# Kernel optimization log

Measured on AMD Instinct MI355X. Metric: run time of the kernel, lower is better.

## Reference

```python
import jax, jax.numpy as jnp
import numpy as np

HIDDEN = 768
HEADS = 12
HEAD_DIM = HIDDEN // HEADS
LN_EPS = 1e-5


def setup_inputs() -> dict:
    key = jax.random.key(0)
    ks = jax.random.split(key, 12)
    B, S, H = 8, 1024, HIDDEN
    s = 1.0 / np.sqrt(H)
    inputs = jax.random.normal(ks[0], (B, S, H), dtype=jnp.float32)
    adj = jax.random.randint(ks[1], (B, S, S), 0, 2, dtype=jnp.int32)
    Wq = jax.random.uniform(ks[2], (H, H), jnp.float32, -s, s)
    bq = jax.random.uniform(ks[3], (H,), jnp.float32, -s, s)
    Wk = jax.random.uniform(ks[4], (H, H), jnp.float32, -s, s)
    bk = jax.random.uniform(ks[5], (H,), jnp.float32, -s, s)
    Wv = jax.random.uniform(ks[6], (H, H), jnp.float32, -s, s)
    bv = jax.random.uniform(ks[7], (H,), jnp.float32, -s, s)
    Wo = jax.random.uniform(ks[8], (H, H), jnp.float32, -s, s)
    bo = jax.random.uniform(ks[9], (H,), jnp.float32, -s, s)
    gamma = jnp.ones((H,), jnp.float32)
    beta = jnp.zeros((H,), jnp.float32)
    return {"inputs": inputs, "adj": adj, "Wq": Wq, "bq": bq, "Wk": Wk,
            "bk": bk, "Wv": Wv, "bv": bv, "Wo": Wo, "bo": bo,
            "gamma": gamma, "beta": beta}


def reference(inputs, adj, Wq, bq, Wk, bk, Wv, bv, Wo, bo, gamma, beta):
    B, S, H = inputs.shape
    def heads(x):  # [B,S,H] -> [B,heads,S,head_dim]
        return x.reshape(B, S, HEADS, HEAD_DIM).transpose(0, 2, 1, 3)
    Q = heads(inputs @ Wq.T + bq)
    K = heads(inputs @ Wk.T + bk)
    V = heads(inputs @ Wv.T + bv)
    scores = jnp.einsum('bhqd,bhkd->bhqk', Q, K) / np.sqrt(HEAD_DIM)
    mask = (adj[:, None, :, :] == 0)  # [B,1,S,S] broadcast over heads
    scores = jnp.where(mask, jnp.float32(-1e9), scores)
    attn = jax.nn.softmax(scores, axis=-1)
    # dropout is identity in eval mode
    ctx = jnp.einsum('bhqk,bhkd->bhqd', attn, V)
    ctx = ctx.transpose(0, 2, 1, 3).reshape(B, S, H)
    out = ctx @ Wo.T + bo
    x = out + inputs
    mu = jnp.mean(x, axis=-1, keepdims=True)
    var = jnp.mean(jnp.square(x - mu), axis=-1, keepdims=True)
    return (x - mu) * jax.lax.rsqrt(var + LN_EPS) * gamma + beta
```

## Files before the change

### kernel.cpp

```cpp
#include <hip/hip_runtime.h>

typedef __bf16 bf16_t;
typedef __bf16 bf16x8 __attribute__((ext_vector_type(8)));
typedef float f32x4 __attribute__((ext_vector_type(4)));
typedef unsigned short u16;

__device__ __forceinline__ u16 f2bf(float f) {
  unsigned u = __float_as_uint(f);
  unsigned r = (u + 0x7fffu + ((u >> 16) & 1u)) >> 16;
  return (u16)r;
}
__device__ __forceinline__ float bf2f(u16 u) {
  return __uint_as_float(((unsigned)u) << 16);
}

typedef const unsigned __attribute__((address_space(1)))* gptr_t;
typedef unsigned __attribute__((address_space(3)))* lptr_t;

__device__ __forceinline__ void gload_lds16(const u16* g, u16* l) {
  __builtin_amdgcn_global_load_lds((gptr_t)(const void*)g, (lptr_t)(void*)l, 16, 0, 0);
}

#define QSCALE 0.18033688f
#define EPS 136

__global__ __launch_bounds__(256) void cvt_f32_bf16(const float* __restrict__ in,
                                                    u16* __restrict__ out, int n4) {
  int i = blockIdx.x * 256 + threadIdx.x;
  if (i >= n4) return;
  float4 v = reinterpret_cast<const float4*>(in)[i];
  ushort4 o;
  o.x = f2bf(v.x); o.y = f2bf(v.y); o.z = f2bf(v.z); o.w = f2bf(v.w);
  reinterpret_cast<ushort4*>(out)[i] = o;
}

__global__ __launch_bounds__(256) void cvt_w4(const float* __restrict__ Wq,
                                              const float* __restrict__ Wk,
                                              const float* __restrict__ Wv,
                                              const float* __restrict__ Wo,
                                              u16* __restrict__ out) {
  int sel = blockIdx.y;
  const float* in = sel == 0 ? Wq : sel == 1 ? Wk : sel == 2 ? Wv : Wo;
  u16* o = out + sel * 589824;
  int i = blockIdx.x * 256 + threadIdx.x;
  float4 v = reinterpret_cast<const float4*>(in)[i];
  ushort4 ov;
  ov.x = f2bf(v.x); ov.y = f2bf(v.y); ov.z = f2bf(v.z); ov.w = f2bf(v.w);
  reinterpret_cast<ushort4*>(o)[i] = ov;
}

__global__ __launch_bounds__(256) void pack_adj(const int* __restrict__ adj,
                                                unsigned* __restrict__ bits) {
  unsigned idx = blockIdx.x * 256u + threadIdx.x;
  int a = adj[idx];
  unsigned long long m = __ballot(a != 0);
  int l = threadIdx.x & 63;
  if ((l & 31) == 0) bits[idx >> 5] = (unsigned)(m >> (l & 32));
}


__global__ __launch_bounds__(256, 4) void gemm_qkv(
    const u16* __restrict__ A,
    const u16* __restrict__ Wq, const u16* __restrict__ Wk, const u16* __restrict__ Wv,
    const float* __restrict__ bq, const float* __restrict__ bk, const float* __restrict__ bv,
    u16* __restrict__ Qo, u16* __restrict__ Ko, u16* __restrict__ Vo) {
  __shared__ u16 lds[2][2][128 * 32];
  const int tid = threadIdx.x;
  const int w = tid >> 6, l = tid & 63;
  const int bm = blockIdx.x;
  const int bn = blockIdx.y;
  const int sel = bn / 6;
  const int bnl = bn % 6;
  const int lr = l & 15, lg = l >> 4;
  const int wm = w >> 1, wn = w & 1;

  const u16* W = sel == 0 ? Wq : sel == 1 ? Wk : Wv;
  const float* bias = sel == 0 ? bq : sel == 1 ? bk : bv;

  const u16* Abase = A + (bm * 128) * 768;
  const u16* Wbase = W + (bnl * 128) * 768;

  const int c0 = tid, c1 = tid + 256;
  const int sr0 = c0 >> 3, pg0 = c0 & 7, g0 = pg0 ^ (sr0 & 7);
  const int off0 = (2 * sr0 + (g0 >> 2)) * 768 + (g0 & 3) * 8;
  const int sr1 = c1 >> 3, pg1 = c1 & 7, g1 = pg1 ^ (sr1 & 7);
  const int off1 = (2 * sr1 + (g1 >> 2)) * 768 + (g1 & 3) * 8;

  int aoff[4], boff[4];
#pragma unroll
  for (int i = 0; i < 4; ++i) {
    int R = wm * 64 + i * 16 + lr, sr = R >> 1;
    int g = (R & 1) * 4 + lg, pg = g ^ (sr & 7);
    aoff[i] = sr * 64 + pg * 8;
    R = wn * 64 + i * 16 + lr; sr = R >> 1;
    g = (R & 1) * 4 + lg; pg = g ^ (sr & 7);
    boff[i] = sr * 64 + pg * 8;
  }

  f32x4 acc[4][4];
#pragma unroll
  for (int i = 0; i < 4; ++i)
#pragma unroll
    for (int j = 0; j < 4; ++j) acc[i][j] = f32x4{0.f, 0.f, 0.f, 0.f};

  auto stage = [&](int buf, int k0) {
    gload_lds16(Abase + off0 + k0, &lds[buf][0][c0 * 8]);
    gload_lds16(Abase + off1 + k0, &lds[buf][0][c1 * 8]);
    gload_lds16(Wbase + off0 + k0, &lds[buf][1][c0 * 8]);
    gload_lds16(Wbase + off1 + k0, &lds[buf][1][c1 * 8]);
  };

  stage(0, 0);
  int cur = 0;
  for (int kt = 0; kt < 24; ++kt) {
    __syncthreads();
    if (kt < 23) stage(cur ^ 1, (kt + 1) * 32);
    const u16* la = &lds[cur][0][0];
    const u16* lb = &lds[cur][1][0];
    bf16x8 af[4], bw[4];
#pragma unroll
    for (int i = 0; i < 4; ++i) af[i] = *(const bf16x8*)&la[aoff[i]];
#pragma unroll
    for (int j = 0; j < 4; ++j) bw[j] = *(const bf16x8*)&lb[boff[j]];
#pragma unroll
    for (int i = 0; i < 4; ++i)
#pragma unroll
      for (int j = 0; j < 4; ++j)
        acc[i][j] = __builtin_amdgcn_mfma_f32_16x16x32_bf16(af[i], bw[j], acc[i][j], 0, 0, 0);
    cur ^= 1;
  }

  __syncthreads();
  u16* ep = &lds[0][0][0];
  const int n0 = bnl * 128 + wn * 64;

  if (sel != 2) {
    const float sc = sel == 0 ? QSCALE : 1.0f;
    u16* dst = sel == 0 ? Qo : Ko;
#pragma unroll
    for (int p = 0; p < 2; ++p) {
      if (wm == p) {
#pragma unroll
        for (int j = 0; j < 4; ++j) {
          float bs = bias[n0 + j * 16 + lr];
#pragma unroll
          for (int i = 0; i < 4; ++i)
#pragma unroll
            for (int r = 0; r < 4; ++r)
              ep[(i * 16 + lg * 4 + r) * EPS + wn * 64 + j * 16 + lr] =
                  f2bf((acc[i][j][r] + bs) * sc);
        }
      }
      __syncthreads();
#pragma unroll
      for (int it = 0; it < 4; ++it) {
        int u = it * 256 + tid, row = u >> 4, cc = u & 15;
        uint4 val = *(const uint4*)&ep[row * EPS + cc * 8];
        int m = bm * 128 + p * 64 + row;
        int b_ = m >> 10, s_ = m & 1023;
        int h_ = (bnl * 128 + cc * 8) >> 6, d_ = (cc & 7) * 8;
        *(uint4*)&dst[((b_ * 12 + h_) * 1024 + s_) * 64 + d_] = val;
      }
      __syncthreads();
    }
  } else {
#pragma unroll
    for (int p = 0; p < 2; ++p) {
      if (wn == p) {
#pragma unroll
        for (int j = 0; j < 4; ++j) {
          float bs = bias[n0 + j * 16 + lr];
#pragma unroll
          for (int i = 0; i < 4; ++i) {
            ushort4 o4;
            o4.x = f2bf(acc[i][j][0] + bs);
            o4.y = f2bf(acc[i][j][1] + bs);
            o4.z = f2bf(acc[i][j][2] + bs);
            o4.w = f2bf(acc[i][j][3] + bs);
            *(ushort4*)&ep[(j * 16 + lr) * EPS + wm * 64 + i * 16 + lg * 4] = o4;
          }
        }
      }
      __syncthreads();
#pragma unroll
      for (int it = 0; it < 4; ++it) {
        int u = it * 256 + tid, row = u >> 4, cc = u & 15;
        uint4 val = *(const uint4*)&ep[row * EPS + cc * 8];
        int dg = bnl * 128 + p * 64 + row;
        int h_ = dg >> 6, d_ = dg & 63;
        int b_ = bm >> 3, s_ = (bm & 7) * 128 + cc * 8;
        *(uint4*)&Vo[((b_ * 12 + h_) * 64 + d_) * 1024 + s_] = val;
      }
      __syncthreads();
    }
  }
}

__global__ __launch_bounds__(256, 4) void gemm_o(
    const u16* __restrict__ A, const u16* __restrict__ W,
    const float* __restrict__ bias, u16* __restrict__ xb) {
  __shared__ u16 lds[2][2][128 * 32];
  const int tid = threadIdx.x;
  const int w = tid >> 6, l = tid & 63;
  const int bm = blockIdx.x, bn = blockIdx.y;
  const int lr = l & 15, lg = l >> 4;
  const int wm = w >> 1, wn = w & 1;

  const u16* Abase = A + (bm * 128) * 768;
  const u16* Wbase = W + (bn * 128) * 768;

  const int c0 = tid, c1 = tid + 256;
  const int sr0 = c0 >> 3, pg0 = c0 & 7, g0 = pg0 ^ (sr0 & 7);
  const int off0 = (2 * sr0 + (g0 >> 2)) * 768 + (g0 & 3) * 8;
  const int sr1 = c1 >> 3, pg1 = c1 & 7, g1 = pg1 ^ (sr1 & 7);
  const int off1 = (2 * sr1 + (g1 >> 2)) * 768 + (g1 & 3) * 8;

  int aoff[4], boff[4];
#pragma unroll
  for (int i = 0; i < 4; ++i) {
    int R = wm * 64 + i * 16 + lr, sr = R >> 1;
    int g = (R & 1) * 4 + lg, pg = g ^ (sr & 7);
    aoff[i] = sr * 64 + pg * 8;
    R = wn * 64 + i * 16 + lr; sr = R >> 1;
    g = (R & 1) * 4 + lg; pg = g ^ (sr & 7);
    boff[i] = sr * 64 + pg * 8;
  }

  f32x4 acc[4][4];
#pragma unroll
  for (int i = 0; i < 4; ++i)
#pragma unroll
    for (int j = 0; j < 4; ++j) acc[i][j] = f32x4{0.f, 0.f, 0.f, 0.f};

  auto stage = [&](int buf, int k0) {
    gload_lds16(Abase + off0 + k0, &lds[buf][0][c0 * 8]);
    gload_lds16(Abase + off1 + k0, &lds[buf][0][c1 * 8]);
    gload_lds16(Wbase + off0 + k0, &lds[buf][1][c0 * 8]);
    gload_lds16(Wbase + off1 + k0, &lds[buf][1][c1 * 8]);
  };

  stage(0, 0);
  int cur = 0;
  for (int kt = 0; kt < 24; ++kt) {
    __syncthreads();
    if (kt < 23) stage(cur ^ 1, (kt + 1) * 32);
    const u16* la = &lds[cur][0][0];
    const u16* lb = &lds[cur][1][0];
    bf16x8 af[4], bw[4];
#pragma unroll
    for (int i = 0; i < 4; ++i) af[i] = *(const bf16x8*)&la[aoff[i]];
#pragma unroll
    for (int j = 0; j < 4; ++j) bw[j] = *(const bf16x8*)&lb[boff[j]];
#pragma unroll
    for (int i = 0; i < 4; ++i)
#pragma unroll
      for (int j = 0; j < 4; ++j)
        acc[i][j] = __builtin_amdgcn_mfma_f32_16x16x32_bf16(af[i], bw[j], acc[i][j], 0, 0, 0);
    cur ^= 1;
  }

  __syncthreads();
  u16* ep = &lds[0][0][0];
  const int n0 = bn * 128 + wn * 64;
#pragma unroll
  for (int p = 0; p < 2; ++p) {
    if (wm == p) {
#pragma unroll
      for (int j = 0; j < 4; ++j) {
        float bs = bias[n0 + j * 16 + lr];
#pragma unroll
        for (int i = 0; i < 4; ++i)
#pragma unroll
          for (int r = 0; r < 4; ++r)
            ep[(i * 16 + lg * 4 + r) * EPS + wn * 64 + j * 16 + lr] =
                f2bf(acc[i][j][r] + bs);
      }
    }
    __syncthreads();
#pragma unroll
    for (int it = 0; it < 4; ++it) {
      int u = it * 256 + tid, row = u >> 4, cc = u & 15;
      uint4 val = *(const uint4*)&ep[row * EPS + cc * 8];
      int m = bm * 128 + p * 64 + row;
      *(uint4*)&xb[m * 768 + bn * 128 + cc * 8] = val;
    }
    __syncthreads();
  }
}

__global__ __launch_bounds__(256) void attn(
    const u16* __restrict__ Q,
    const u16* __restrict__ Kt,
    const u16* __restrict__ VT,
    const unsigned* __restrict__ bits,
    u16* __restrict__ ctx) {
  __shared__ u16 kl[2][64 * 64];
  __shared__ u16 vl[2][64 * 64];
  __shared__ __bf16 plds_all[4][16 * 64];
  const int tid = threadIdx.x;
  const int w = tid >> 6, l = tid & 63;
  const int lr = l & 15, lg = l >> 4;
  const int bh = blockIdx.x;
  const int qt = (blockIdx.y << 2) | w;
  const int b_ = bh / 12, h_ = bh % 12;
  __bf16* plds = plds_all[w];

  const u16* Qb = Q + (bh * 1024 + qt * 16) * 64;
  const u16* Kb = Kt + bh * 1024 * 64;
  const u16* Vb = VT + bh * 64 * 1024;
  const unsigned* wb = bits + (b_ * 1024 + qt * 16) * 32;

  bf16x8 qa0 = *(const bf16x8*)&Qb[lr * 64 + lg * 8];
  bf16x8 qa1 = *(const bf16x8*)&Qb[lr * 64 + 32 + lg * 8];

  bf16x8 vones;
#pragma unroll
  for (int i = 0; i < 8; ++i) vones[i] = (__bf16)1.0f;

  f32x4 cacc[4];
#pragma unroll
  for (int j = 0; j < 4; ++j) cacc[j] = f32x4{0.f, 0.f, 0.f, 0.f};
  f32x4 lacc = f32x4{0.f, 0.f, 0.f, 0.f};

  auto stage = [&](int buf, int k0) {
#pragma unroll
    for (int j = 0; j < 2; ++j) {
      const int seg = j * 4 + w;
      const int c = seg * 64 + l;
      const int row = c >> 3, g = c & 7;
      const int gp = ((g ^ (row & 7)) << 3);
      gload_lds16(Kb + (k0 + row) * 64 + gp, &kl[buf][seg * 512]);
      gload_lds16(Vb + row * 1024 + k0 + gp, &vl[buf][seg * 512]);
    }
  };

  stage(0, 0);
  __syncthreads();
  int cur = 0;

  for (int kt = 0; kt < 16; ++kt) {
    const int k0 = kt * 64;
    if (kt < 15) stage(cur ^ 1, k0 + 64);

    uint2 mm[4];
#pragma unroll
    for (int r = 0; r < 4; ++r)
      mm[r] = *(const uint2*)&wb[(lg * 4 + r) * 32 + kt * 2];

    f32x4 s[4];
#pragma unroll
    for (int t = 0; t < 4; ++t) {
      const int row = t * 16 + lr;
      const int sw = row & 7;
      bf16x8 ka = *(const bf16x8*)&kl[cur][row * 64 + ((lg ^ sw) << 3)];
      bf16x8 kb2 = *(const bf16x8*)&kl[cur][row * 64 + (((4 + lg) ^ sw) << 3)];
      f32x4 z = f32x4{0.f, 0.f, 0.f, 0.f};
      z = __builtin_amdgcn_mfma_f32_16x16x32_bf16(qa0, ka, z, 0, 0, 0);
      z = __builtin_amdgcn_mfma_f32_16x16x32_bf16(qa1, kb2, z, 0, 0, 0);
      s[t] = z;
    }

#pragma unroll
    for (int r = 0; r < 4; ++r) {
      const int q = lg * 4 + r;
      const int sw = (q & 7) << 3;
      unsigned w0 = mm[r].x >> lr;
      unsigned w1 = mm[r].y >> lr;
#pragma unroll
      for (int t = 0; t < 4; ++t) {
        unsigned bit = (t == 0) ? (w0 & 1u)
                     : (t == 1) ? ((w0 >> 16) & 1u)
                     : (t == 2) ? (w1 & 1u)
                                : ((w1 >> 16) & 1u);
        float sv = bit ? s[t][r] : -1e30f;
        plds[q * 64 + ((t * 16 + lr) ^ sw)] = (__bf16)exp2f(sv);
      }
    }
    asm volatile("s_waitcnt lgkmcnt(0)" ::: "memory");
    const int swr = (lr & 7) << 3;
    bf16x8 pa0 = *(const bf16x8*)&plds[lr * 64 + ((lg * 8) ^ swr)];
    bf16x8 pa1 = *(const bf16x8*)&plds[lr * 64 + ((32 + lg * 8) ^ swr)];

    __builtin_amdgcn_s_setprio(1);
    lacc = __builtin_amdgcn_mfma_f32_16x16x32_bf16(pa0, vones, lacc, 0, 0, 0);
    lacc = __builtin_amdgcn_mfma_f32_16x16x32_bf16(pa1, vones, lacc, 0, 0, 0);
#pragma unroll
    for (int j = 0; j < 4; ++j) {
      const int row = j * 16 + lr;
      const int sw = row & 7;
      bf16x8 v0 = *(const bf16x8*)&vl[cur][row * 64 + ((lg ^ sw) << 3)];
      bf16x8 v1 = *(const bf16x8*)&vl[cur][row * 64 + (((4 + lg) ^ sw) << 3)];
      cacc[j] = __builtin_amdgcn_mfma_f32_16x16x32_bf16(pa0, v0, cacc[j], 0, 0, 0);
      cacc[j] = __builtin_amdgcn_mfma_f32_16x16x32_bf16(pa1, v1, cacc[j], 0, 0, 0);
    }
    __builtin_amdgcn_s_setprio(0);

    __syncthreads();
    cur ^= 1;
  }

  float inv[4];
#pragma unroll
  for (int r = 0; r < 4; ++r) inv[r] = 1.0f / lacc[r];
#pragma unroll
  for (int j = 0; j < 4; ++j) {
#pragma unroll
    for (int r = 0; r < 4; ++r) {
      int q = qt * 16 + lg * 4 + r;
      ctx[(b_ * 1024 + q) * 768 + h_ * 64 + j * 16 + lr] = f2bf(cacc[j][r] * inv[r]);
    }
  }
}

__global__ __launch_bounds__(256) void layernorm(const u16* __restrict__ xb,
                                                 const float* __restrict__ resid,
                                                 const float* __restrict__ gamma,
                                                 const float* __restrict__ beta,
                                                 float* __restrict__ out) {
  int row = blockIdx.x * 4 + (threadIdx.x >> 6);
  int l = threadIdx.x & 63;
  const ushort4* xr = (const ushort4*)(xb + row * 768);
  const float4* rr = (const float4*)(resid + row * 768);
  float v[12];
  float s = 0.f;
#pragma unroll
  for (int c = 0; c < 3; ++c) {
    ushort4 xs = xr[l + c * 64];
    float4 rv = rr[l + c * 64];
    v[c * 4 + 0] = bf2f(xs.x) + rv.x;
    v[c * 4 + 1] = bf2f(xs.y) + rv.y;
    v[c * 4 + 2] = bf2f(xs.z) + rv.z;
    v[c * 4 + 3] = bf2f(xs.w) + rv.w;
    s += v[c * 4 + 0] + v[c * 4 + 1] + v[c * 4 + 2] + v[c * 4 + 3];
  }
#pragma unroll
  for (int d = 1; d < 64; d <<= 1) s += __shfl_xor(s, d);
  float mu = s * (1.0f / 768.0f);
  float vs = 0.f;
#pragma unroll
  for (int k = 0; k < 12; ++k) {
    float q = v[k] - mu;
    vs += q * q;
  }
#pragma unroll
  for (int d = 1; d < 64; d <<= 1) vs += __shfl_xor(vs, d);
  float rs = rsqrtf(vs * (1.0f / 768.0f) + 1e-5f);
  const float4* g4 = (const float4*)gamma;
  const float4* b4 = (const float4*)beta;
#pragma unroll
  for (int c = 0; c < 3; ++c) {
    float4 g = g4[l + c * 64], bb = b4[l + c * 64];
    float4 o;
    o.x = (v[c * 4 + 0] - mu) * rs * g.x + bb.x;
    o.y = (v[c * 4 + 1] - mu) * rs * g.y + bb.y;
    o.z = (v[c * 4 + 2] - mu) * rs * g.z + bb.z;
    o.w = (v[c * 4 + 3] - mu) * rs * g.w + bb.w;
    ((float4*)(out + row * 768))[l + c * 64] = o;
  }
}

extern "C" void kernel_launch(void* const* d_in, const int* in_sizes, int n_in,
                              void* d_out, int out_size, void* d_ws, size_t ws_size,
                              hipStream_t stream) {
  (void)in_sizes; (void)n_in; (void)out_size; (void)ws_size;
  const float* inputs = (const float*)d_in[0];
  const int* adj = (const int*)d_in[1];
  const float* Wq = (const float*)d_in[2];
  const float* bq = (const float*)d_in[3];
  const float* Wk = (const float*)d_in[4];
  const float* bk = (const float*)d_in[5];
  const float* Wv = (const float*)d_in[6];
  const float* bv = (const float*)d_in[7];
  const float* Wo = (const float*)d_in[8];
  const float* bo = (const float*)d_in[9];
  const float* gamma = (const float*)d_in[10];
  const float* beta = (const float*)d_in[11];
  float* out = (float*)d_out;
  char* ws = (char*)d_ws;

  u16* Xbf = (u16*)(ws + 0);
  u16* Wqb = (u16*)(ws + 12582912);
  u16* Wkb = (u16*)(ws + 13762560);
  u16* Wvb = (u16*)(ws + 14942208);
  u16* Wob = (u16*)(ws + 16121856);
  u16* Qb  = (u16*)(ws + 17301504);
  u16* Kb  = (u16*)(ws + 29884416);
  u16* VTb = (u16*)(ws + 42467328);
  unsigned* bits = (unsigned*)(ws + 55050240);
  u16* ctxb = (u16*)(ws + 0);
  u16* xb = (u16*)(ws + 17301504);

  cvt_f32_bf16<<<6144, 256, 0, stream>>>(inputs, Xbf, 1572864);
  cvt_w4<<<dim3(576, 4), 256, 0, stream>>>(Wq, Wk, Wv, Wo, Wqb);
  pack_adj<<<32768, 256, 0, stream>>>(adj, bits);

  gemm_qkv<<<dim3(64, 18), 256, 0, stream>>>(Xbf, Wqb, Wkb, Wvb, bq, bk, bv, Qb, Kb, VTb);

  attn<<<dim3(96, 16), 256, 0, stream>>>(Qb, Kb, VTb, bits, ctxb);

  gemm_o<<<dim3(64, 6), 256, 0, stream>>>(ctxb, Wob, bo, xb);

  layernorm<<<2048, 256, 0, stream>>>(xb, inputs, gamma, beta, out);
}
```

Measured before the change: 255.1 us.

## Fuse prep kernels and transpose score MFMA for packed P writes

Merges the three preprocessing kernels (input cast, weight cast, adjacency bit-packing) into one launch with block-range dispatch, removing two kernel launches. In attention, swaps the MFMA operands so each lane holds four consecutive key scores for one query. That lets it load a single mask word per lane, use the hardware exp2 intrinsic, and write packed bf16 pairs to LDS as 8-byte stores instead of scalar 2-byte stores. LDS offsets are also hoisted out of the loop. Masked entries now become exact zeros rather than exp2 of a large negative value.

```diff
diff --git a/kernel.cpp b/kernel.cpp
--- a/kernel.cpp
+++ b/kernel.cpp
@@ -13,6 +13,11 @@
 __device__ __forceinline__ float bf2f(u16 u) {
   return __uint_as_float(((unsigned)u) << 16);
 }
+__device__ __forceinline__ unsigned pk2(float a, float b) {
+  unsigned lo = __builtin_bit_cast(unsigned short, (__bf16)a);
+  unsigned hi = __builtin_bit_cast(unsigned short, (__bf16)b);
+  return lo | (hi << 16);
+}
 
 typedef const unsigned __attribute__((address_space(1)))* gptr_t;
 typedef unsigned __attribute__((address_space(3)))* lptr_t;
@@ -24,38 +29,35 @@
 #define QSCALE 0.18033688f
 #define EPS 136
 
-__global__ __launch_bounds__(256) void cvt_f32_bf16(const float* __restrict__ in,
-                                                    u16* __restrict__ out, int n4) {
-  int i = blockIdx.x * 256 + threadIdx.x;
-  if (i >= n4) return;
-  float4 v = reinterpret_cast<const float4*>(in)[i];
-  ushort4 o;
-  o.x = f2bf(v.x); o.y = f2bf(v.y); o.z = f2bf(v.z); o.w = f2bf(v.w);
-  reinterpret_cast<ushort4*>(out)[i] = o;
-}
-
-__global__ __launch_bounds__(256) void cvt_w4(const float* __restrict__ Wq,
-                                              const float* __restrict__ Wk,
-                                              const float* __restrict__ Wv,
-                                              const float* __restrict__ Wo,
-                                              u16* __restrict__ out) {
-  int sel = blockIdx.y;
-  const float* in = sel == 0 ? Wq : sel == 1 ? Wk : sel == 2 ? Wv : Wo;
-  u16* o = out + sel * 589824;
-  int i = blockIdx.x * 256 + threadIdx.x;
-  float4 v = reinterpret_cast<const float4*>(in)[i];
-  ushort4 ov;
-  ov.x = f2bf(v.x); ov.y = f2bf(v.y); ov.z = f2bf(v.z); ov.w = f2bf(v.w);
-  reinterpret_cast<ushort4*>(o)[i] = ov;
-}
-
-__global__ __launch_bounds__(256) void pack_adj(const int* __restrict__ adj,
-                                                unsigned* __restrict__ bits) {
-  unsigned idx = blockIdx.x * 256u + threadIdx.x;
-  int a = adj[idx];
-  unsigned long long m = __ballot(a != 0);
-  int l = threadIdx.x & 63;
-  if ((l & 31) == 0) bits[idx >> 5] = (unsigned)(m >> (l & 32));
+__global__ __launch_bounds__(256) void prep(
+    const float* __restrict__ inputs, const float* __restrict__ Wq,
+    const float* __restrict__ Wk, const float* __restrict__ Wv,
+    const float* __restrict__ Wo, const int* __restrict__ adj,
+    u16* __restrict__ Xbf, u16* __restrict__ Wall, unsigned* __restrict__ bits) {
+  const int bid = blockIdx.x;
+  const int tid = threadIdx.x;
+  if (bid < 6144) {
+    int i = bid * 256 + tid;
+    float4 v = reinterpret_cast<const float4*>(inputs)[i];
+    ushort4 o;
+    o.x = f2bf(v.x); o.y = f2bf(v.y); o.z = f2bf(v.z); o.w = f2bf(v.w);
+    reinterpret_cast<ushort4*>(Xbf)[i] = o;
+  } else if (bid < 8448) {
+    int b2 = bid - 6144;
+    int sel = b2 / 576;
+    const float* in = sel == 0 ? Wq : sel == 1 ? Wk : sel == 2 ? Wv : Wo;
+    int i = (b2 % 576) * 256 + tid;
+    float4 v = reinterpret_cast<const float4*>(in)[i];
+    ushort4 o;
+    o.x = f2bf(v.x); o.y = f2bf(v.y); o.z = f2bf(v.z); o.w = f2bf(v.w);
+    reinterpret_cast<ushort4*>(Wall + sel * 589824)[i] = o;
+  } else {
+    unsigned idx = (bid - 8448) * 256u + tid;
+    int a = adj[idx];
+    unsigned long long m = __ballot(a != 0);
+    int l = tid & 63;
+    if ((l & 31) == 0) bits[idx >> 5] = (unsigned)(m >> (l & 32));
+  }
 }
 
 
@@ -296,19 +298,19 @@
     u16* __restrict__ ctx) {
   __shared__ u16 kl[2][64 * 64];
   __shared__ u16 vl[2][64 * 64];
-  __shared__ __bf16 plds_all[4][16 * 64];
+  __shared__ unsigned plds_all[4][16 * 32];
   const int tid = threadIdx.x;
   const int w = tid >> 6, l = tid & 63;
   const int lr = l & 15, lg = l >> 4;
   const int bh = blockIdx.x;
   const int qt = (blockIdx.y << 2) | w;
   const int b_ = bh / 12, h_ = bh % 12;
-  __bf16* plds = plds_all[w];
+  unsigned* plds = plds_all[w];
 
   const u16* Qb = Q + (bh * 1024 + qt * 16) * 64;
   const u16* Kb = Kt + bh * 1024 * 64;
   const u16* Vb = VT + bh * 64 * 1024;
-  const unsigned* wb = bits + (b_ * 1024 + qt * 16) * 32;
+  const unsigned* wbq = bits + (b_ * 1024 + qt * 16) * 32 + lr * 32;
 
   bf16x8 qa0 = *(const bf16x8*)&Qb[lr * 64 + lg * 8];
   bf16x8 qa1 = *(const bf16x8*)&Qb[lr * 64 + 32 + lg * 8];
@@ -316,6 +318,21 @@
   bf16x8 vones;
 #pragma unroll
   for (int i = 0; i < 8; ++i) vones[i] = (__bf16)1.0f;
+
+  const int sw2 = (lr & 7) << 2;
+  int off[4][2];
+#pragma unroll
+  for (int t = 0; t < 4; ++t) {
+    const int row = t * 16 + lr, sw = row & 7;
+    off[t][0] = row * 64 + ((lg ^ sw) << 3);
+    off[t][1] = row * 64 + (((4 + lg) ^ sw) << 3);
+  }
+  int pw[4];
+#pragma unroll
+  for (int t = 0; t < 4; ++t) pw[t] = lr * 32 + ((t * 8 + 2 * lg) ^ sw2);
+  const int pr0 = lr * 32 + ((lg * 4) ^ sw2);
+  const int pr1 = lr * 32 + ((16 + lg * 4) ^ sw2);
+  const int sh = lg * 4;
 
   f32x4 cacc[4];
 #pragma unroll
@@ -339,57 +356,47 @@
   int cur = 0;
 
   for (int kt = 0; kt < 16; ++kt) {
-    const int k0 = kt * 64;
-    if (kt < 15) stage(cur ^ 1, k0 + 64);
-
-    uint2 mm[4];
-#pragma unroll
-    for (int r = 0; r < 4; ++r)
-      mm[r] = *(const uint2*)&wb[(lg * 4 + r) * 32 + kt * 2];
+    if (kt < 15) stage(cur ^ 1, (kt + 1) * 64);
+
+    uint2 mmq = *(const uint2*)&wbq[kt * 2];
+    unsigned u0 = mmq.x >> sh;
+    unsigned u1 = mmq.y >> sh;
 
     f32x4 s[4];
 #pragma unroll
     for (int t = 0; t < 4; ++t) {
-      const int row = t * 16 + lr;
-      const int sw = row & 7;
-      bf16x8 ka = *(const bf16x8*)&kl[cur][row * 64 + ((lg ^ sw) << 3)];
-      bf16x8 kb2 = *(const bf16x8*)&kl[cur][row * 64 + (((4 + lg) ^ sw) << 3)];
+      bf16x8 ka = *(const bf16x8*)&kl[cur][off[t][0]];
+      bf16x8 kb2 = *(const bf16x8*)&kl[cur][off[t][1]];
       f32x4 z = f32x4{0.f, 0.f, 0.f, 0.f};
-      z = __builtin_amdgcn_mfma_f32_16x16x32_bf16(qa0, ka, z, 0, 0, 0);
-      z = __builtin_amdgcn_mfma_f32_16x16x32_bf16(qa1, kb2, z, 0, 0, 0);
+      z = __builtin_amdgcn_mfma_f32_16x16x32_bf16(ka, qa0, z, 0, 0, 0);
+      z = __builtin_amdgcn_mfma_f32_16x16x32_bf16(kb2, qa1, z, 0, 0, 0);
       s[t] = z;
     }
 
 #pragma unroll
-    for (int r = 0; r < 4; ++r) {
-      const int q = lg * 4 + r;
-      const int sw = (q & 7) << 3;
-      unsigned w0 = mm[r].x >> lr;
-      unsigned w1 = mm[r].y >> lr;
-#pragma unroll
-      for (int t = 0; t < 4; ++t) {
-        unsigned bit = (t == 0) ? (w0 & 1u)
-                     : (t == 1) ? ((w0 >> 16) & 1u)
-                     : (t == 2) ? (w1 & 1u)
-                                : ((w1 >> 16) & 1u);
-        float sv = bit ? s[t][r] : -1e30f;
-        plds[q * 64 + ((t * 16 + lr) ^ sw)] = (__bf16)exp2f(sv);
-      }
+    for (int t = 0; t < 4; ++t) {
+      const unsigned uw = (t < 2) ? u0 : u1;
+      const int bsh = (t & 1) * 16;
+      float p0 = ((uw >> (bsh + 0)) & 1u) ? __builtin_amdgcn_exp2f(s[t][0]) : 0.f;
+      float p1 = ((uw >> (bsh + 1)) & 1u) ? __builtin_amdgcn_exp2f(s[t][1]) : 0.f;
+      float p2 = ((uw >> (bsh + 2)) & 1u) ? __builtin_amdgcn_exp2f(s[t][2]) : 0.f;
+      float p3 = ((uw >> (bsh + 3)) & 1u) ? __builtin_amdgcn_exp2f(s[t][3]) : 0.f;
+      uint2 pkd;
+      pkd.x = pk2(p0, p1);
+      pkd.y = pk2(p2, p3);
+      *(uint2*)&plds[pw[t]] = pkd;
     }
     asm volatile("s_waitcnt lgkmcnt(0)" ::: "memory");
-    const int swr = (lr & 7) << 3;
-    bf16x8 pa0 = *(const bf16x8*)&plds[lr * 64 + ((lg * 8) ^ swr)];
-    bf16x8 pa1 = *(const bf16x8*)&plds[lr * 64 + ((32 + lg * 8) ^ swr)];
+    bf16x8 pa0 = *(const bf16x8*)&plds[pr0];
+    bf16x8 pa1 = *(const bf16x8*)&plds[pr1];
 
     __builtin_amdgcn_s_setprio(1);
     lacc = __builtin_amdgcn_mfma_f32_16x16x32_bf16(pa0, vones, lacc, 0, 0, 0);
     lacc = __builtin_amdgcn_mfma_f32_16x16x32_bf16(pa1, vones, lacc, 0, 0, 0);
 #pragma unroll
     for (int j = 0; j < 4; ++j) {
-      const int row = j * 16 + lr;
-      const int sw = row & 7;
-      bf16x8 v0 = *(const bf16x8*)&vl[cur][row * 64 + ((lg ^ sw) << 3)];
-      bf16x8 v1 = *(const bf16x8*)&vl[cur][row * 64 + (((4 + lg) ^ sw) << 3)];
+      bf16x8 v0 = *(const bf16x8*)&vl[cur][off[j][0]];
+      bf16x8 v1 = *(const bf16x8*)&vl[cur][off[j][1]];
       cacc[j] = __builtin_amdgcn_mfma_f32_16x16x32_bf16(pa0, v0, cacc[j], 0, 0, 0);
       cacc[j] = __builtin_amdgcn_mfma_f32_16x16x32_bf16(pa1, v1, cacc[j], 0, 0, 0);
     }
@@ -490,9 +497,7 @@
   u16* ctxb = (u16*)(ws + 0);
   u16* xb = (u16*)(ws + 17301504);
 
-  cvt_f32_bf16<<<6144, 256, 0, stream>>>(inputs, Xbf, 1572864);
-  cvt_w4<<<dim3(576, 4), 256, 0, stream>>>(Wq, Wk, Wv, Wo, Wqb);
-  pack_adj<<<32768, 256, 0, stream>>>(adj, bits);
+  prep<<<41216, 256, 0, stream>>>(inputs, Wq, Wk, Wv, Wo, adj, Xbf, Wqb, bits);
 
   gemm_qkv<<<dim3(64, 18), 256, 0, stream>>>(Xbf, Wqb, Wkb, Wvb, bq, bk, bv, Qb, Kb, VTb);
 
```

Result: faster. 245.2 us (-3.9%).
